# Kernel optimization log

Measured on AMD Instinct MI355X. Metric: run time of the kernel, lower is better.

The kernel has to match this reference:

```python
import jax, jax.numpy as jnp
import numpy as np

B, K, D, H = 32768, 16, 256, 2
HD = D // H
LN_EPS = 1e-5


def setup_inputs() -> dict:
    key = jax.random.key(0)
    ks = jax.random.split(key, 10)
    s = 1.0 / np.sqrt(D)
    return {
        "center_emb": jax.random.normal(ks[0], (B, D), dtype=jnp.float32),
        "neighbor_embs": jax.random.normal(ks[1], (B, K, D), dtype=jnp.float32),
        "edge_weights": jax.random.uniform(ks[2], (B, K), dtype=jnp.float32),
        "Wq": jax.random.uniform(ks[3], (D, D), jnp.float32, -s, s),
        "Wk": jax.random.uniform(ks[4], (D, D), jnp.float32, -s, s),
        "Wv": jax.random.uniform(ks[5], (D, D), jnp.float32, -s, s),
        "Wc": jax.random.uniform(ks[6], (D // 2, D), jnp.float32, -s, s),
        "Wx": jax.random.uniform(ks[7], (D // 2, D), jnp.float32, -s, s),
        "ln_gamma": jnp.ones((D,), jnp.float32),
        "ln_beta": jnp.zeros((D,), jnp.float32),
    }


def reference(center_emb, neighbor_embs, edge_weights, Wq, Wk, Wv, Wc, Wx, ln_gamma, ln_beta):
    scale = HD ** -0.5
    # projections (nn.Linear: x @ W.T)
    q = (center_emb @ Wq.T).reshape(B, H, HD)          # [B,H,hd]
    k = (neighbor_embs @ Wk.T).reshape(B, K, H, HD)    # [B,K,H,hd]
    v = (neighbor_embs @ Wv.T).reshape(B, K, H, HD)
    # attention scores with additive edge-weight topology bias
    scores = jnp.einsum("bhd,bkhd->bhk", q, k) * scale + edge_weights[:, None, :]
    attn = jax.nn.softmax(scores, axis=-1)             # [B,H,K] (dropout: eval mode)
    context = jnp.einsum("bhk,bkhd->bhd", attn, v).reshape(B, D)
    # LayerNorm over D
    mu = jnp.mean(context, axis=-1, keepdims=True)
    var = jnp.var(context, axis=-1, keepdims=True)
    ctx_n = (context - mu) * jax.lax.rsqrt(var + LN_EPS) * ln_gamma + ln_beta
    # concat of center / context half-projections
    return jnp.concatenate([center_emb @ Wc.T, ctx_n @ Wx.T], axis=-1)
```

## Files before the change

kernel.cpp:

```cpp
#include <hip/hip_runtime.h>

#define Bsz 32768
#define BR  32
#define SCALE 0.08838834764831845f

typedef __attribute__((ext_vector_type(4))) float f32x4;
typedef __attribute__((ext_vector_type(4))) unsigned short us4;
typedef __attribute__((ext_vector_type(8))) unsigned short us8;
typedef __attribute__((ext_vector_type(4))) unsigned int ui4;
typedef __attribute__((ext_vector_type(2))) unsigned int ui2;
typedef _Float16 __attribute__((ext_vector_type(2))) h2;
typedef _Float16 __attribute__((ext_vector_type(8))) h8;

static __device__ __forceinline__ unsigned int pk16(float a, float b){
  return __builtin_bit_cast(unsigned int, __builtin_amdgcn_cvt_pkrtz(a, b));
}
static __device__ __forceinline__ h2 uph(unsigned int u){
  return __builtin_bit_cast(h2, u);
}
static __device__ __forceinline__ float h2f(unsigned short h){
  return (float)__builtin_bit_cast(_Float16, h);
}
static __device__ __forceinline__ unsigned short f16b(float x){
  return __builtin_bit_cast(unsigned short, (_Float16)x);
}
static __device__ __forceinline__ h8 ldh8(const unsigned short* p){
  return __builtin_bit_cast(h8, *(const us8*)p);
}
#define FDOT2(a, b, c) __builtin_amdgcn_fdot2((a), (b), (c), false)
#define MFMA16(a, b, c) __builtin_amdgcn_mfma_f32_16x16x32_f16((a), (b), (c), 0, 0, 0)

__global__ void prep_kernel(const float* __restrict__ Wq, const float* __restrict__ Wk,
                            const float* __restrict__ Wv, const float* __restrict__ Wc,
                            const float* __restrict__ Wx, unsigned short* __restrict__ wsp){
  unsigned short* W1R = wsp;
  unsigned int*   W2P = (unsigned int*)(wsp + 640*256);
  unsigned int*   W3P = W2P + 128*256;
  const int n = blockIdx.x;
  const int k = threadIdx.x;
  float val;
  if (n < 512){
    const int h = n >> 8, m = n & 255;
    const float* wq = Wq + h*128*256 + k;
    const float* wk = Wk + h*128*256 + m;
    float s = 0.f;
    for (int d = 0; d < 128; ++d) s += wq[d*256] * wk[d*256];
    val = s;
  } else if (n < 640){
    val = Wc[(n-512)*256 + k];
  } else if (n < 896){
    val = Wv[(n-640)*256 + k];
  } else {
    val = Wx[(n-896)*256 + k];
  }
  if (n < 640){
    W1R[n*256 + k] = f16b(val);
  } else {
    const float vo = __shfl_xor(val, 1, 64);
    if ((k & 1) == 0){
      const unsigned int p = pk16(val, vo);
      const int kp = k >> 1;
      if (n < 896) W2P[kp*256 + (n-640)] = p;
      else         W3P[kp*128 + (n-896)] = p;
    }
  }
}

__global__ __launch_bounds__(256, 4) void fused_kernel(
    const float* __restrict__ center, const float* __restrict__ nbr,
    const float* __restrict__ ew, const float* __restrict__ gamma,
    const float* __restrict__ beta, const unsigned short* __restrict__ Wall,
    float* __restrict__ out)
{
  __shared__ __align__(16) unsigned short s_ctil[BR*520];

  const int tid  = threadIdx.x;
  const int wid  = tid >> 6;
  const int lane = tid & 63;
  const int b0   = blockIdx.x * BR;

  const unsigned short* W1R = Wall;
  const unsigned int*   W2P = (const unsigned int*)(Wall + 640*256);
  const unsigned int*   W3P = W2P + 128*256;

  const int rt = tid >> 5;
  const int ct = tid & 31;

  {
    const int sr = tid >> 3;
    const int fc = (tid & 7) * 32;
    const float* cp = center + ((long)(b0 + sr) << 8) + fc;
    #pragma unroll
    for (int it = 0; it < 4; ++it){
      float4 a = *(const float4*)(cp + it*8);
      float4 b = *(const float4*)(cp + it*8 + 4);
      ui4 v = {pk16(a.x,a.y), pk16(a.z,a.w), pk16(b.x,b.y), pk16(b.z,b.w)};
      *(ui4*)&s_ctil[sr*520 + 256 + fc + it*8] = v;
    }
  }
  __syncthreads();

  {
    const int rowg = wid >> 1;
    const int colh = wid & 1;
    const int l15 = lane & 15, lq = lane >> 4;
    h8 af[8];
    #pragma unroll
    for (int kk = 0; kk < 8; ++kk)
      af[kk] = __builtin_bit_cast(h8,
        *(const us8*)&s_ctil[(rowg*16 + l15)*520 + 256 + kk*32 + lq*8]);
    __syncthreads();
    #pragma unroll 1
    for (int c0t = 0; c0t < 20; c0t += 5){
      f32x4 acc[5];
      #pragma unroll
      for (int u = 0; u < 5; ++u) acc[u] = (f32x4){0,0,0,0};
      #pragma unroll
      for (int kk = 0; kk < 8; ++kk)
        #pragma unroll
        for (int u = 0; u < 5; ++u){
          const int gt = colh*20 + c0t + u;
          acc[u] = MFMA16(af[kk], ldh8(W1R + (gt*16 + l15)*256 + kk*32 + lq*8), acc[u]);
        }
      #pragma unroll
      for (int u = 0; u < 5; ++u){
        const int gt = colh*20 + c0t + u;
        if (gt < 32){
          #pragma unroll
          for (int j = 0; j < 4; ++j)
            s_ctil[(rowg*16 + lq*4 + j)*520 + gt*16 + l15] = f16b(acc[u][j]);
        } else {
          #pragma unroll
          for (int j = 0; j < 4; ++j)
            out[((long)(b0 + rowg*16 + lq*4 + j) << 8) + (gt-32)*16 + l15] = acc[u][j];
        }
      }
    }
  }
  __syncthreads();

  {
    const int myk = ((lane>>4)&1)*8 + ((lane>>3)&1)*4 + ((lane>>2)&1)*2 + ((lane>>1)&1);
    const int myh = lane >> 5;
    #pragma unroll 1
    for (int rr = 0; rr < 8; ++rr){
      const int r = wid*8 + rr;
      const long b = b0 + r;
      float4 c0, c1;
      {
        us4 h0 = *(const us4*)&s_ctil[r*520 + lane*4];
        us4 h1 = *(const us4*)&s_ctil[r*520 + 256 + lane*4];
        c0.x=h2f(h0[0]); c0.y=h2f(h0[1]); c0.z=h2f(h0[2]); c0.w=h2f(h0[3]);
        c1.x=h2f(h1[0]); c1.y=h2f(h1[1]); c1.z=h2f(h1[2]); c1.w=h2f(h1[3]);
      }
      float4 xv[16];
      const float* npt = nbr + ((b << 4) << 8) + lane*4;
      #pragma unroll
      for (int k = 0; k < 16; ++k) xv[k] = *(const float4*)(npt + (k << 8));
      float P0[16], P1[16];
      #pragma unroll
      for (int k = 0; k < 16; ++k){
        P0[k] = xv[k].x*c0.x + xv[k].y*c0.y + xv[k].z*c0.z + xv[k].w*c0.w;
        P1[k] = xv[k].x*c1.x + xv[k].y*c1.y + xv[k].z*c1.z + xv[k].w*c1.w;
      }
      const int b5 = lane & 32, b4 = lane & 16, b3 = lane & 8, b2 = lane & 4, b1 = lane & 2;
      float Q[16];
      #pragma unroll
      for (int j = 0; j < 16; ++j){
        const float give = b5 ? P0[j] : P1[j];
        const float keep = b5 ? P1[j] : P0[j];
        Q[j] = keep + __shfl_xor(give, 32, 64);
      }
      float R[8];
      #pragma unroll
      for (int j = 0; j < 8; ++j){
        const float give = b4 ? Q[j] : Q[8+j];
        const float keep = b4 ? Q[8+j] : Q[j];
        R[j] = keep + __shfl_xor(give, 16, 64);
      }
      float S[4];
      #pragma unroll
      for (int j = 0; j < 4; ++j){
        const float give = b3 ? R[j] : R[4+j];
        const float keep = b3 ? R[4+j] : R[j];
        S[j] = keep + __shfl_xor(give, 8, 64);
      }
      float T[2];
      #pragma unroll
      for (int j = 0; j < 2; ++j){
        const float give = b2 ? S[j] : S[2+j];
        const float keep = b2 ? S[2+j] : S[j];
        T[j] = keep + __shfl_xor(give, 4, 64);
      }
      float U;
      {
        const float give = b1 ? T[0] : T[1];
        const float keep = b1 ? T[1] : T[0];
        U = keep + __shfl_xor(give, 2, 64);
      }
      const float sfull = U + __shfl_xor(U, 1, 64);
      const float erk = ew[b*16 + myk];
      const float e = __expf(sfull*SCALE + erk);
      float dn = e;
      dn += __shfl_xor(dn, 2, 64);
      dn += __shfl_xor(dn, 4, 64);
      dn += __shfl_xor(dn, 8, 64);
      dn += __shfl_xor(dn, 16, 64);
      const float w = e / dn;
      float* wbuf = (float*)&s_ctil[r*520 + 256];
      wbuf[myh*16 + myk] = w;
      f32x4 wv[8];
      #pragma unroll
      for (int t = 0; t < 8; ++t) wv[t] = ((const f32x4*)wbuf)[t];
      float4 agg0 = {0,0,0,0}, agg1 = {0,0,0,0};
      #pragma unroll
      for (int k = 0; k < 16; ++k){
        const float w0 = wv[k>>2][k&3];
        const float w1 = wv[4 + (k>>2)][k&3];
        agg0.x += w0*xv[k].x; agg0.y += w0*xv[k].y; agg0.z += w0*xv[k].z; agg0.w += w0*xv[k].w;
        agg1.x += w1*xv[k].x; agg1.y += w1*xv[k].y; agg1.z += w1*xv[k].z; agg1.w += w1*xv[k].w;
      }
      ui2 v0 = {pk16(agg0.x, agg0.y), pk16(agg0.z, agg0.w)};
      ui2 v1 = {pk16(agg1.x, agg1.y), pk16(agg1.z, agg1.w)};
      *(ui2*)&s_ctil[r*520 + lane*4]       = v0;
      *(ui2*)&s_ctil[r*520 + 256 + lane*4] = v1;
    }
  }

  {
    f32x4 cacc[4][2];
    #pragma unroll
    for (int rr = 0; rr < 4; ++rr){ cacc[rr][0] = (f32x4){0,0,0,0}; cacc[rr][1] = (f32x4){0,0,0,0}; }
    #pragma unroll 1
    for (int k0 = 0; k0 < 256; k0 += 8){
      ui4 a0[4], a1[4];
      #pragma unroll
      for (int rr = 0; rr < 4; ++rr){
        a0[rr] = *(const ui4*)&s_ctil[(4*rt+rr)*520 + k0];
        a1[rr] = *(const ui4*)&s_ctil[(4*rt+rr)*520 + 256 + k0];
      }
      #pragma unroll
      for (int kp = 0; kp < 4; ++kp){
        const unsigned int* wrow = W2P + ((k0>>1) + kp)*256;
        const ui4 w0 = ((const ui4*)(wrow      ))[ct];
        const ui4 w1 = ((const ui4*)(wrow + 128))[ct];
        #pragma unroll
        for (int rr = 0; rr < 4; ++rr){
          const h2 x0 = uph(a0[rr][kp]);
          const h2 x1 = uph(a1[rr][kp]);
          #pragma unroll
          for (int j = 0; j < 4; ++j){
            cacc[rr][0][j] = FDOT2(x0, uph(w0[j]), cacc[rr][0][j]);
            cacc[rr][1][j] = FDOT2(x1, uph(w1[j]), cacc[rr][1][j]);
          }
        }
      }
    }
    const f32x4 gv0 = ((const f32x4*)gamma)[ct], gv1 = ((const f32x4*)gamma)[32 + ct];
    const f32x4 bv0 = ((const f32x4*)beta )[ct], bv1 = ((const f32x4*)beta )[32 + ct];
    #pragma unroll
    for (int rr = 0; rr < 4; ++rr){
      float s = 0.f, q = 0.f;
      #pragma unroll
      for (int t = 0; t < 2; ++t)
        #pragma unroll
        for (int j = 0; j < 4; ++j){
          const float x = cacc[rr][t][j];
          s += x; q += x*x;
        }
      #pragma unroll
      for (int m = 16; m >= 1; m >>= 1){
        s += __shfl_xor(s, m, 64);
        q += __shfl_xor(q, m, 64);
      }
      const float mu  = s * (1.f/256.f);
      const float var = q * (1.f/256.f) - mu*mu;
      const float rs  = rsqrtf(var + 1e-5f);
      const int r = 4*rt + rr;
      float y0[4], y1[4];
      #pragma unroll
      for (int j = 0; j < 4; ++j){
        y0[j] = (cacc[rr][0][j] - mu)*rs*gv0[j] + bv0[j];
        y1[j] = (cacc[rr][1][j] - mu)*rs*gv1[j] + bv1[j];
      }
      ui2 v0 = {pk16(y0[0], y0[1]), pk16(y0[2], y0[3])};
      ui2 v1 = {pk16(y1[0], y1[1]), pk16(y1[2], y1[3])};
      *(ui2*)&s_ctil[r*520 + ct*4]       = v0;
      *(ui2*)&s_ctil[r*520 + 128 + ct*4] = v1;
    }
  }

  {
    f32x4 eacc[4];
    #pragma unroll
    for (int rr = 0; rr < 4; ++rr) eacc[rr] = (f32x4){0,0,0,0};
    #pragma unroll 1
    for (int k0 = 0; k0 < 256; k0 += 8){
      ui4 a8[4];
      #pragma unroll
      for (int rr = 0; rr < 4; ++rr)
        a8[rr] = *(const ui4*)&s_ctil[(4*rt+rr)*520 + k0];
      #pragma unroll
      for (int kp = 0; kp < 4; ++kp){
        const ui4 w = ((const ui4*)(W3P + ((k0>>1) + kp)*128))[ct];
        #pragma unroll
        for (int rr = 0; rr < 4; ++rr){
          const h2 x = uph(a8[rr][kp]);
          #pragma unroll
          for (int j = 0; j < 4; ++j)
            eacc[rr][j] = FDOT2(x, uph(w[j]), eacc[rr][j]);
        }
      }
    }
    #pragma unroll
    for (int rr = 0; rr < 4; ++rr)
      *(f32x4*)&out[((long)(b0 + 4*rt + rr) << 8) + 128 + ct*4] = eacc[rr];
  }
}

extern "C" void kernel_launch(void* const* d_in, const int* in_sizes, int n_in,
                              void* d_out, int out_size, void* d_ws, size_t ws_size,
                              hipStream_t stream){
  const float* center = (const float*)d_in[0];
  const float* nbr    = (const float*)d_in[1];
  const float* ew     = (const float*)d_in[2];
  const float* Wq     = (const float*)d_in[3];
  const float* Wk     = (const float*)d_in[4];
  const float* Wv     = (const float*)d_in[5];
  const float* Wc     = (const float*)d_in[6];
  const float* Wx     = (const float*)d_in[7];
  const float* gamma  = (const float*)d_in[8];
  const float* beta   = (const float*)d_in[9];
  (void)in_sizes; (void)n_in; (void)out_size;

  unsigned short* W = (unsigned short*)d_ws;
  (void)ws_size;

  prep_kernel<<<1024, 256, 0, stream>>>(Wq, Wk, Wv, Wc, Wx, W);
  fused_kernel<<<Bsz/BR, 256, 0, stream>>>(center, nbr, ew, gamma, beta, W, (float*)d_out);
}
```

Before: 219.3 us.

## Compute Wv projection and LayerNorm stage with MFMA instead of fdot2

Replaces the FDOT2-based value-projection GEMM (per-head aggregated neighbors times Wv) with 16x16x32 f16 MFMA instructions, reading Wv as a row-major f16 matrix directly from global memory. The prep kernel now stores Wv row-major instead of k-pair packed. LayerNorm statistics are reduced with lane shuffles, and because each wave now covers only half the columns, partial sums are exchanged between wave pairs through shared memory. This adds extra block barriers and scalar f16 shared stores in exchange for using the matrix cores on this stage.

```diff
diff --git a/kernel.cpp b/kernel.cpp
--- a/kernel.cpp
+++ b/kernel.cpp
@@ -34,8 +34,8 @@
                             const float* __restrict__ Wv, const float* __restrict__ Wc,
                             const float* __restrict__ Wx, unsigned short* __restrict__ wsp){
   unsigned short* W1R = wsp;
-  unsigned int*   W2P = (unsigned int*)(wsp + 640*256);
-  unsigned int*   W3P = W2P + 128*256;
+  unsigned short* W2R = wsp + 640*256;
+  unsigned int*   W3P = (unsigned int*)(wsp + 640*256 + 256*256);
   const int n = blockIdx.x;
   const int k = threadIdx.x;
   float val;
@@ -55,14 +55,12 @@
   }
   if (n < 640){
     W1R[n*256 + k] = f16b(val);
+  } else if (n < 896){
+    W2R[(n-640)*256 + k] = f16b(val);
   } else {
     const float vo = __shfl_xor(val, 1, 64);
-    if ((k & 1) == 0){
-      const unsigned int p = pk16(val, vo);
-      const int kp = k >> 1;
-      if (n < 896) W2P[kp*256 + (n-640)] = p;
-      else         W3P[kp*128 + (n-896)] = p;
-    }
+    if ((k & 1) == 0)
+      W3P[(k >> 1)*128 + (n-896)] = pk16(val, vo);
   }
 }
 
@@ -80,8 +78,8 @@
   const int b0   = blockIdx.x * BR;
 
   const unsigned short* W1R = Wall;
-  const unsigned int*   W2P = (const unsigned int*)(Wall + 640*256);
-  const unsigned int*   W3P = W2P + 128*256;
+  const unsigned short* W2R = Wall + 640*256;
+  const unsigned int*   W3P = (const unsigned int*)(Wall + 640*256 + 256*256);
 
   const int rt = tid >> 5;
   const int ct = tid & 31;
@@ -226,69 +224,74 @@
       *(ui2*)&s_ctil[r*520 + 256 + lane*4] = v1;
     }
   }
-
-  {
-    f32x4 cacc[4][2];
-    #pragma unroll
-    for (int rr = 0; rr < 4; ++rr){ cacc[rr][0] = (f32x4){0,0,0,0}; cacc[rr][1] = (f32x4){0,0,0,0}; }
-    #pragma unroll 1
-    for (int k0 = 0; k0 < 256; k0 += 8){
-      ui4 a0[4], a1[4];
-      #pragma unroll
-      for (int rr = 0; rr < 4; ++rr){
-        a0[rr] = *(const ui4*)&s_ctil[(4*rt+rr)*520 + k0];
-        a1[rr] = *(const ui4*)&s_ctil[(4*rt+rr)*520 + 256 + k0];
-      }
-      #pragma unroll
-      for (int kp = 0; kp < 4; ++kp){
-        const unsigned int* wrow = W2P + ((k0>>1) + kp)*256;
-        const ui4 w0 = ((const ui4*)(wrow      ))[ct];
-        const ui4 w1 = ((const ui4*)(wrow + 128))[ct];
-        #pragma unroll
-        for (int rr = 0; rr < 4; ++rr){
-          const h2 x0 = uph(a0[rr][kp]);
-          const h2 x1 = uph(a1[rr][kp]);
-          #pragma unroll
-          for (int j = 0; j < 4; ++j){
-            cacc[rr][0][j] = FDOT2(x0, uph(w0[j]), cacc[rr][0][j]);
-            cacc[rr][1][j] = FDOT2(x1, uph(w1[j]), cacc[rr][1][j]);
-          }
-        }
-      }
-    }
-    const f32x4 gv0 = ((const f32x4*)gamma)[ct], gv1 = ((const f32x4*)gamma)[32 + ct];
-    const f32x4 bv0 = ((const f32x4*)beta )[ct], bv1 = ((const f32x4*)beta )[32 + ct];
-    #pragma unroll
-    for (int rr = 0; rr < 4; ++rr){
-      float s = 0.f, q = 0.f;
-      #pragma unroll
-      for (int t = 0; t < 2; ++t)
-        #pragma unroll
-        for (int j = 0; j < 4; ++j){
-          const float x = cacc[rr][t][j];
-          s += x; q += x*x;
-        }
-      #pragma unroll
-      for (int m = 16; m >= 1; m >>= 1){
-        s += __shfl_xor(s, m, 64);
-        q += __shfl_xor(q, m, 64);
-      }
-      const float mu  = s * (1.f/256.f);
-      const float var = q * (1.f/256.f) - mu*mu;
+  __syncthreads();
+
+  {
+    const int rowg = wid >> 1;
+    const int colh = wid & 1;
+    const int l15 = lane & 15, lq = lane >> 4;
+    h8 cf[8];
+    #pragma unroll
+    for (int kk = 0; kk < 8; ++kk)
+      cf[kk] = __builtin_bit_cast(h8,
+        *(const us8*)&s_ctil[(rowg*16 + l15)*520 + colh*256 + kk*32 + lq*8]);
+    f32x4 cacc[8];
+    #pragma unroll
+    for (int t = 0; t < 8; ++t) cacc[t] = (f32x4){0,0,0,0};
+    #pragma unroll
+    for (int kk = 0; kk < 8; ++kk)
+      #pragma unroll
+      for (int t = 0; t < 8; ++t){
+        const int col = colh*128 + t*16 + l15;
+        cacc[t] = MFMA16(cf[kk], ldh8(W2R + col*256 + kk*32 + lq*8), cacc[t]);
+      }
+    float ps[4], pq[4];
+    #pragma unroll
+    for (int j = 0; j < 4; ++j){
+      float sm = 0.f, qm = 0.f;
+      #pragma unroll
+      for (int t = 0; t < 8; ++t){ const float x = cacc[t][j]; sm += x; qm += x*x; }
+      #pragma unroll
+      for (int m = 1; m <= 8; m <<= 1){
+        sm += __shfl_xor(sm, m, 64);
+        qm += __shfl_xor(qm, m, 64);
+      }
+      ps[j] = sm; pq[j] = qm;
+    }
+    __syncthreads();
+    if (l15 == 0){
+      #pragma unroll
+      for (int j = 0; j < 4; ++j){
+        float* pp = (float*)&s_ctil[(rowg*16 + lq*4 + j)*520 + 256];
+        pp[colh*2]     = ps[j];
+        pp[colh*2 + 1] = pq[j];
+      }
+    }
+    __syncthreads();
+    float gv[8], bv[8];
+    #pragma unroll
+    for (int t = 0; t < 8; ++t){
+      const int col = colh*128 + t*16 + l15;
+      gv[t] = gamma[col];
+      bv[t] = beta[col];
+    }
+    #pragma unroll
+    for (int j = 0; j < 4; ++j){
+      const int r = rowg*16 + lq*4 + j;
+      const float* pp = (const float*)&s_ctil[r*520 + 256];
+      const float sm = pp[0] + pp[2];
+      const float qm = pp[1] + pp[3];
+      const float mu  = sm * (1.f/256.f);
+      const float var = qm * (1.f/256.f) - mu*mu;
       const float rs  = rsqrtf(var + 1e-5f);
-      const int r = 4*rt + rr;
-      float y0[4], y1[4];
-      #pragma unroll
-      for (int j = 0; j < 4; ++j){
-        y0[j] = (cacc[rr][0][j] - mu)*rs*gv0[j] + bv0[j];
-        y1[j] = (cacc[rr][1][j] - mu)*rs*gv1[j] + bv1[j];
-      }
-      ui2 v0 = {pk16(y0[0], y0[1]), pk16(y0[2], y0[3])};
-      ui2 v1 = {pk16(y1[0], y1[1]), pk16(y1[2], y1[3])};
-      *(ui2*)&s_ctil[r*520 + ct*4]       = v0;
-      *(ui2*)&s_ctil[r*520 + 128 + ct*4] = v1;
-    }
-  }
+      #pragma unroll
+      for (int t = 0; t < 8; ++t){
+        const int col = colh*128 + t*16 + l15;
+        s_ctil[r*520 + col] = f16b((cacc[t][j] - mu)*rs*gv[t] + bv[t]);
+      }
+    }
+  }
+  __syncthreads();
 
   {
     f32x4 eacc[4];
```

Measured after the change: 212.4 us. 3.1% less time.
